# Performance work log

Hardware: AMD Instinct MI355X
Metric: run time of the kernel (lower is better)

## Reference

```python
import math
import jax, jax.numpy as jnp
import numpy as np

EMBED_DIM = 768
NUM_HEADS = 12
SCALE = 0.125
KERNEL_SIZE = 5
SIGMA = 1.0


def gaussian_kernel1d(ksize, sigma):
    x = jnp.arange(ksize, dtype=jnp.float32) - (ksize - 1) / 2.0
    g = jnp.exp(-0.5 * (x / sigma) ** 2)
    return g / g.sum()


def gaussian_blur_2d(x, ksize, sigma):
    # x: [N, C, P, P]; per-channel (depthwise) separable gaussian blur,
    # reflect padding, matching torchvision.transforms.functional.gaussian_blur.
    N, C, P, _ = x.shape
    g = gaussian_kernel1d(ksize, sigma)
    k2d = jnp.outer(g, g)[None, None]  # [1,1,k,k] (separable == full outer kernel)
    pad = ksize // 2
    xp = jnp.pad(x.reshape(N * C, 1, P, P), ((0, 0), (0, 0), (pad, pad), (pad, pad)), mode='reflect')
    y = jax.lax.conv_general_dilated(
        xp, k2d.astype(x.dtype), window_strides=(1, 1), padding='VALID',
        dimension_numbers=('NCHW', 'OIHW', 'NCHW'))
    return y.reshape(N, C, P, P)


def setup_inputs() -> dict:
    key = jax.random.key(0)
    k1, k2 = jax.random.split(key)
    B, S, E = 8, 1024, EMBED_DIM
    x = jax.random.normal(k1, (B, S, E), dtype=jnp.float32)
    # xavier_uniform for [3E, E]
    bound = math.sqrt(6.0 / (3 * E + E))
    W_in = jax.random.uniform(k2, (3 * E, E), dtype=jnp.float32, minval=-bound, maxval=bound)
    return {"x": x, "W_in": W_in}


def reference(x, W_in):
    B, S, E = x.shape
    H, D = NUM_HEADS, E // NUM_HEADS
    # fused QKV projection; chunk order is (values, keys, queries)
    qkv = jnp.einsum('bse,fe->bsf', x, W_in)  # [B, S, 3E]
    _v, k, q = jnp.split(qkv, 3, axis=-1)

    def to_heads(t):
        return t.reshape(B, S, H, D).transpose(0, 2, 1, 3).reshape(B * H, S, D)

    q, k = to_heads(q), to_heads(k)
    logits = SCALE * jnp.einsum('nqd,nkd->nqk', q, k)  # [B*H, S, S]
    P = int(math.sqrt(S))
    logits4 = logits.reshape(B * H, S, P, P)  # key axis viewed as PxP patch grid
    blurred = gaussian_blur_2d(logits4, KERNEL_SIZE, SIGMA)
    attn = jax.nn.softmax(blurred.reshape(B * H, S, S), axis=-1)
    return attn
```

## Files before the change

### kernel.cpp

```cpp
#include <hip/hip_runtime.h>


typedef __attribute__((ext_vector_type(8))) short short8;
typedef __attribute__((ext_vector_type(4))) float f32x4;

__device__ __forceinline__ float bf2f(unsigned short u) {
    unsigned int v = ((unsigned int)u) << 16;
    return __builtin_bit_cast(float, v);
}
__device__ __forceinline__ unsigned short f2bf(float f) {
    unsigned int u = __builtin_bit_cast(unsigned int, f);
    u += 0x7FFFu + ((u >> 16) & 1u);
    return (unsigned short)(u >> 16);
}

__device__ __forceinline__ void g2lds16(const unsigned short* g, unsigned short* l) {
    __builtin_amdgcn_global_load_lds(
        (const __attribute__((address_space(1))) void*)g,
        (__attribute__((address_space(3))) void*)l, 16, 0, 0);
}

#if defined(__has_builtin) && __has_builtin(__builtin_amdgcn_exp2f)
#define EXP2F(x) __builtin_amdgcn_exp2f(x)
#else
#define EXP2F(x) exp2f(x)
#endif

#define QSCALE 0.1803368801111204f

__global__ __launch_bounds__(256) void k_cast(const float* __restrict__ x,
                                              const float* __restrict__ w,
                                              unsigned short* __restrict__ dst) {
    const int NX = 8 * 1024 * 768;
    int i = (blockIdx.x * 256 + threadIdx.x) * 4;
    float4 v;
    if (i < NX) v = *(const float4*)(x + i);
    else        v = *(const float4*)(w + 768 * 768 + (i - NX));
    ushort4 o;
    o.x = f2bf(v.x); o.y = f2bf(v.y); o.z = f2bf(v.z); o.w = f2bf(v.w);
    *(ushort4*)(dst + i) = o;
}

__global__ __launch_bounds__(256) void k_proj(const unsigned short* __restrict__ xb,
                                              const unsigned short* __restrict__ wb,
                                              unsigned short* __restrict__ qh,
                                              unsigned short* __restrict__ kh) {
    __shared__ unsigned short As[128 * 64];
    __shared__ unsigned short Bs[128 * 64];

    const int lane = threadIdx.x & 63;
    const int wv   = threadIdx.x >> 6;
    const int m0   = blockIdx.x * 128;
    const int n0   = blockIdx.y * 128;
    const int col  = lane & 15;
    const int quad = lane >> 4;
    const int wm   = (wv >> 1) * 64;
    const int wn   = (wv & 1) * 64;

    const int srow   = wv * 32 + (lane >> 3);
    const int schunk = ((lane & 7) ^ ((lane >> 3) & 7)) * 8;
    const unsigned short* ag = xb + (size_t)(m0 + srow) * 768 + schunk;
    const unsigned short* bg = wb + (size_t)(n0 + srow) * 768 + schunk;
    unsigned short* al = As + (wv * 32) * 64;
    unsigned short* bl = Bs + (wv * 32) * 64;

    f32x4 acc[4][4] = {};

    for (int kk = 0; kk < 768; kk += 64) {
        __syncthreads();
#pragma unroll
        for (int j = 0; j < 4; ++j) {
            g2lds16(ag + j * 8 * 768 + kk, al + j * 8 * 64);
            g2lds16(bg + j * 8 * 768 + kk, bl + j * 8 * 64);
        }
        __syncthreads();

#pragma unroll
        for (int kc = 0; kc < 2; ++kc) {
            const int ch = ((kc * 4 + quad) ^ (col & 7)) * 8;
            short8 a[4], b[4];
#pragma unroll
            for (int mt = 0; mt < 4; ++mt)
                a[mt] = *(const short8*)(const void*)(As + (wm + mt * 16 + col) * 64 + ch);
#pragma unroll
            for (int nt = 0; nt < 4; ++nt)
                b[nt] = *(const short8*)(const void*)(Bs + (wn + nt * 16 + col) * 64 + ch);
#pragma unroll
            for (int mt = 0; mt < 4; ++mt)
#pragma unroll
                for (int nt = 0; nt < 4; ++nt)
                    acc[mt][nt] = __builtin_amdgcn_mfma_f32_16x16x32_bf16(
                        a[mt], b[nt], acc[mt][nt], 0, 0, 0);
        }
    }

#pragma unroll
    for (int nt = 0; nt < 4; ++nt) {
        int f = n0 + wn + nt * 16 + col;
        bool isq = (f >= 768);
        int fl = isq ? (f - 768) : f;
        int h = fl >> 6, d = fl & 63;
        unsigned short* dstb = isq ? qh : kh;
        float scl = isq ? QSCALE : 1.0f;
#pragma unroll
        for (int mt = 0; mt < 4; ++mt) {
#pragma unroll
            for (int i = 0; i < 4; ++i) {
                int t = m0 + wm + mt * 16 + quad * 4 + i;
                int n = (t >> 10) * 12 + h;
                dstb[((n << 10) + (t & 1023)) * 64 + d] = f2bf(acc[mt][nt][i] * scl);
            }
        }
    }
}

__global__ __launch_bounds__(256) void k_blurf(const unsigned short* __restrict__ src,
                                               unsigned short* __restrict__ dst) {
    __shared__ __align__(16) unsigned short sin_[12 * 32 * 16];
    __shared__ __align__(16) unsigned short stm_[8 * 32 * 16];

    const int tid = threadIdx.x;
    const int n   = blockIdx.y;
    const int rt  = blockIdx.x & 3;
    const int dc  = (blockIdx.x >> 2) * 16;
    const int r0  = rt * 8;
    const float g5[5] = {0.054488684f, 0.24420134f, 0.40261995f, 0.24420134f, 0.054488684f};

#pragma unroll
    for (int it = 0; it < 6; ++it) {
        int l   = it * 256 + tid;
        int row = l >> 7;
        int c   = (l >> 2) & 31;
        int gq  = l & 3;
        int pr  = r0 + row - 2;
        if (pr < 0)  pr = -pr;
        if (pr > 31) pr = 62 - pr;
        *(uint2*)(void*)(sin_ + ((row * 32 + c) << 4) + gq * 4) =
            *(const uint2*)(const void*)(src + (((size_t)n << 10) + pr * 32 + c) * 64 + dc + gq * 4);
    }
    __syncthreads();

#pragma unroll
    for (int it = 0; it < 4; ++it) {
        int l   = it * 256 + tid;
        int row = l >> 7;
        int c   = (l >> 2) & 31;
        int gq  = l & 3;
        float a0 = 0.f, a1 = 0.f, a2 = 0.f, a3 = 0.f;
#pragma unroll
        for (int o = 0; o < 5; ++o) {
            uint2 u = *(const uint2*)(const void*)(sin_ + (((row + o) * 32 + c) << 4) + gq * 4);
            float w = g5[o];
            a0 += w * bf2f((unsigned short)(u.x & 0xffff));
            a1 += w * bf2f((unsigned short)(u.x >> 16));
            a2 += w * bf2f((unsigned short)(u.y & 0xffff));
            a3 += w * bf2f((unsigned short)(u.y >> 16));
        }
        uint2 ov;
        ov.x = (unsigned)f2bf(a0) | ((unsigned)f2bf(a1) << 16);
        ov.y = (unsigned)f2bf(a2) | ((unsigned)f2bf(a3) << 16);
        *(uint2*)(void*)(stm_ + ((row * 32 + c) << 4) + gq * 4) = ov;
    }
    __syncthreads();

#pragma unroll
    for (int it = 0; it < 4; ++it) {
        int l   = it * 256 + tid;
        int row = l >> 7;
        int c   = (l >> 2) & 31;
        int gq  = l & 3;
        float a0 = 0.f, a1 = 0.f, a2 = 0.f, a3 = 0.f;
#pragma unroll
        for (int o = -2; o <= 2; ++o) {
            int pc = c + o;
            if (pc < 0)  pc = -pc;
            if (pc > 31) pc = 62 - pc;
            uint2 u = *(const uint2*)(const void*)(stm_ + ((row * 32 + pc) << 4) + gq * 4);
            float w = g5[o + 2];
            a0 += w * bf2f((unsigned short)(u.x & 0xffff));
            a1 += w * bf2f((unsigned short)(u.x >> 16));
            a2 += w * bf2f((unsigned short)(u.y & 0xffff));
            a3 += w * bf2f((unsigned short)(u.y >> 16));
        }
        uint2 ov;
        ov.x = (unsigned)f2bf(a0) | ((unsigned)f2bf(a1) << 16);
        ov.y = (unsigned)f2bf(a2) | ((unsigned)f2bf(a3) << 16);
        *(uint2*)(void*)(dst + (((size_t)n << 10) + (r0 + row) * 32 + c) * 64 + dc + gq * 4) = ov;
    }
}

__global__ __launch_bounds__(256) void k_attn(const unsigned short* __restrict__ qh,
                                              const unsigned short* __restrict__ kt,
                                              float* __restrict__ out) {
    const int lane = threadIdx.x & 63;
    const int wv   = threadIdx.x >> 6;
    const int n    = blockIdx.y;
    const int s0   = blockIdx.x * 16;
    const int col  = lane & 15;
    const int kq   = (lane >> 4) * 8;

    __shared__ float red[2][4][16];

    const unsigned short* qp = qh + ((n << 10) + s0 + col) * 64 + kq;
    short8 a0 = *(const short8*)(const void*)(qp);
    short8 a1 = *(const short8*)(const void*)(qp + 32);

    f32x4 acc[16];
    const unsigned short* kp = kt + ((n << 10) + wv * 256 + col) * 64 + kq;
#pragma unroll
    for (int t = 0; t < 16; ++t) {
        short8 b0 = *(const short8*)(const void*)(kp + t * 1024);
        short8 b1 = *(const short8*)(const void*)(kp + t * 1024 + 32);
        f32x4 c = {};
        c = __builtin_amdgcn_mfma_f32_16x16x32_bf16(a0, b0, c, 0, 0, 0);
        c = __builtin_amdgcn_mfma_f32_16x16x32_bf16(a1, b1, c, 0, 0, 0);
        acc[t] = c;
    }

    float mx[4];
#pragma unroll
    for (int i = 0; i < 4; ++i) {
        float m = acc[0][i];
#pragma unroll
        for (int t = 1; t < 16; ++t) m = fmaxf(m, acc[t][i]);
#pragma unroll
        for (int off = 1; off < 16; off <<= 1) m = fmaxf(m, __shfl_xor(m, off, 64));
        mx[i] = m;
    }
    if (col == 0) {
#pragma unroll
        for (int i = 0; i < 4; ++i) red[0][wv][(lane >> 4) * 4 + i] = mx[i];
    }
    __syncthreads();

    float sm[4];
#pragma unroll
    for (int i = 0; i < 4; ++i) {
        int qloc = (lane >> 4) * 4 + i;
        float m = fmaxf(fmaxf(red[0][0][qloc], red[0][1][qloc]),
                        fmaxf(red[0][2][qloc], red[0][3][qloc]));
        float s = 0.f;
#pragma unroll
        for (int t = 0; t < 16; ++t) {
            float e = EXP2F(acc[t][i] - m);
            acc[t][i] = e;
            s += e;
        }
#pragma unroll
        for (int off = 1; off < 16; off <<= 1) s += __shfl_xor(s, off, 64);
        sm[i] = s;
    }
    if (col == 0) {
#pragma unroll
        for (int i = 0; i < 4; ++i) red[1][wv][(lane >> 4) * 4 + i] = sm[i];
    }
    __syncthreads();

#pragma unroll
    for (int i = 0; i < 4; ++i) {
        int qloc = (lane >> 4) * 4 + i;
        float s = red[1][0][qloc] + red[1][1][qloc] + red[1][2][qloc] + red[1][3][qloc];
        float inv = 1.0f / s;
        float* op = out + (((size_t)(n << 10) + s0 + qloc) << 10) + wv * 256 + col;
#pragma unroll
        for (int t = 0; t < 16; ++t) op[t * 16] = acc[t][i] * inv;
    }
}

extern "C" void kernel_launch(void* const* d_in, const int* in_sizes, int n_in,
                              void* d_out, int out_size, void* d_ws, size_t ws_size,
                              hipStream_t stream) {
    const float* x = (const float*)d_in[0];
    const float* W = (const float*)d_in[1];
    float* out = (float*)d_out;

    unsigned short* ws   = (unsigned short*)d_ws;
    unsigned short* xb   = ws;
    unsigned short* wb   = xb + 6291456;
    unsigned short* qh   = wb + 1179648;
    unsigned short* kh   = qh + 6291456;
    unsigned short* kt   = kh + 6291456;

    k_cast<<<7296, 256, 0, stream>>>(x, W, xb);
    k_proj<<<dim3(64, 12), 256, 0, stream>>>(xb, wb, qh, kh);
    k_blurf<<<dim3(16, 96), 256, 0, stream>>>(kh, kt);
    k_attn<<<dim3(64, 96), 256, 0, stream>>>(qh, kt, out);
}
```

Baseline: 522.8 us.

## Fuse four kernels into one cooperative persistent kernel with grid syncs

Merges the cast, QKV projection, blur and attention/softmax kernels into a single cooperative kernel launched with 768 blocks. Stages are separated by grid-wide syncs, and blocks loop over the work of the blur and attention stages. This is meant to remove per-launch overhead and the gaps between kernels. In exchange it adds grid-sync cost, caps occupancy at 768 resident blocks (launch_bounds 256,3), and keeps the four-launch path as a fallback if the cooperative launch fails.

```diff
diff --git a/kernel.cpp b/kernel.cpp
--- a/kernel.cpp
+++ b/kernel.cpp
@@ -1,4 +1,7 @@
 #include <hip/hip_runtime.h>
+#include <hip/hip_cooperative_groups.h>
+
+namespace cg = cooperative_groups;
 
 
 typedef __attribute__((ext_vector_type(8))) short short8;
@@ -28,11 +31,11 @@
 
 #define QSCALE 0.1803368801111204f
 
-__global__ __launch_bounds__(256) void k_cast(const float* __restrict__ x,
-                                              const float* __restrict__ w,
-                                              unsigned short* __restrict__ dst) {
+
+__device__ __forceinline__ void cast_body(int i, const float* __restrict__ x,
+                                          const float* __restrict__ w,
+                                          unsigned short* __restrict__ dst) {
     const int NX = 8 * 1024 * 768;
-    int i = (blockIdx.x * 256 + threadIdx.x) * 4;
     float4 v;
     if (i < NX) v = *(const float4*)(x + i);
     else        v = *(const float4*)(w + 768 * 768 + (i - NX));
@@ -41,17 +44,16 @@
     *(ushort4*)(dst + i) = o;
 }
 
-__global__ __launch_bounds__(256) void k_proj(const unsigned short* __restrict__ xb,
-                                              const unsigned short* __restrict__ wb,
-                                              unsigned short* __restrict__ qh,
-                                              unsigned short* __restrict__ kh) {
-    __shared__ unsigned short As[128 * 64];
-    __shared__ unsigned short Bs[128 * 64];
-
-    const int lane = threadIdx.x & 63;
-    const int wv   = threadIdx.x >> 6;
-    const int m0   = blockIdx.x * 128;
-    const int n0   = blockIdx.y * 128;
+__device__ __forceinline__ void proj_body(int bx, int by, int tid,
+                                          unsigned short* As, unsigned short* Bs,
+                                          const unsigned short* __restrict__ xb,
+                                          const unsigned short* __restrict__ wb,
+                                          unsigned short* __restrict__ qh,
+                                          unsigned short* __restrict__ kh) {
+    const int lane = tid & 63;
+    const int wv   = tid >> 6;
+    const int m0   = bx * 128;
+    const int n0   = by * 128;
     const int col  = lane & 15;
     const int quad = lane >> 4;
     const int wm   = (wv >> 1) * 64;
@@ -114,15 +116,12 @@
     }
 }
 
-__global__ __launch_bounds__(256) void k_blurf(const unsigned short* __restrict__ src,
-                                               unsigned short* __restrict__ dst) {
-    __shared__ __align__(16) unsigned short sin_[12 * 32 * 16];
-    __shared__ __align__(16) unsigned short stm_[8 * 32 * 16];
-
-    const int tid = threadIdx.x;
-    const int n   = blockIdx.y;
-    const int rt  = blockIdx.x & 3;
-    const int dc  = (blockIdx.x >> 2) * 16;
+__device__ __forceinline__ void blur_body(int bxx, int n, int tid,
+                                          unsigned short* sin_, unsigned short* stm_,
+                                          const unsigned short* __restrict__ src,
+                                          unsigned short* __restrict__ dst) {
+    const int rt  = bxx & 3;
+    const int dc  = (bxx >> 2) * 16;
     const int r0  = rt * 8;
     const float g5[5] = {0.054488684f, 0.24420134f, 0.40261995f, 0.24420134f, 0.054488684f};
 
@@ -189,17 +188,17 @@
     }
 }
 
-__global__ __launch_bounds__(256) void k_attn(const unsigned short* __restrict__ qh,
-                                              const unsigned short* __restrict__ kt,
-                                              float* __restrict__ out) {
-    const int lane = threadIdx.x & 63;
-    const int wv   = threadIdx.x >> 6;
-    const int n    = blockIdx.y;
-    const int s0   = blockIdx.x * 16;
+__device__ __forceinline__ void attn_body(int s0, int n, int tid,
+                                          float* redf,
+                                          const unsigned short* __restrict__ qh,
+                                          const unsigned short* __restrict__ kt,
+                                          float* __restrict__ out) {
+    const int lane = tid & 63;
+    const int wv   = tid >> 6;
     const int col  = lane & 15;
     const int kq   = (lane >> 4) * 8;
 
-    __shared__ float red[2][4][16];
+#define RED(a, b, c) redf[((a) * 4 + (b)) * 16 + (c)]
 
     const unsigned short* qp = qh + ((n << 10) + s0 + col) * 64 + kq;
     short8 a0 = *(const short8*)(const void*)(qp);
@@ -229,7 +228,7 @@
     }
     if (col == 0) {
 #pragma unroll
-        for (int i = 0; i < 4; ++i) red[0][wv][(lane >> 4) * 4 + i] = mx[i];
+        for (int i = 0; i < 4; ++i) RED(0, wv, (lane >> 4) * 4 + i) = mx[i];
     }
     __syncthreads();
 
@@ -237,8 +236,8 @@
 #pragma unroll
     for (int i = 0; i < 4; ++i) {
         int qloc = (lane >> 4) * 4 + i;
-        float m = fmaxf(fmaxf(red[0][0][qloc], red[0][1][qloc]),
-                        fmaxf(red[0][2][qloc], red[0][3][qloc]));
+        float m = fmaxf(fmaxf(RED(0, 0, qloc), RED(0, 1, qloc)),
+                        fmaxf(RED(0, 2, qloc), RED(0, 3, qloc)));
         float s = 0.f;
 #pragma unroll
         for (int t = 0; t < 16; ++t) {
@@ -252,19 +251,85 @@
     }
     if (col == 0) {
 #pragma unroll
-        for (int i = 0; i < 4; ++i) red[1][wv][(lane >> 4) * 4 + i] = sm[i];
+        for (int i = 0; i < 4; ++i) RED(1, wv, (lane >> 4) * 4 + i) = sm[i];
     }
     __syncthreads();
 
 #pragma unroll
     for (int i = 0; i < 4; ++i) {
         int qloc = (lane >> 4) * 4 + i;
-        float s = red[1][0][qloc] + red[1][1][qloc] + red[1][2][qloc] + red[1][3][qloc];
+        float s = RED(1, 0, qloc) + RED(1, 1, qloc) + RED(1, 2, qloc) + RED(1, 3, qloc);
         float inv = 1.0f / s;
         float* op = out + (((size_t)(n << 10) + s0 + qloc) << 10) + wv * 256 + col;
 #pragma unroll
         for (int t = 0; t < 16; ++t) op[t * 16] = acc[t][i] * inv;
     }
+#undef RED
+}
+
+__global__ __launch_bounds__(256, 3) void k_mega(const float* __restrict__ x,
+                                                 const float* __restrict__ W,
+                                                 unsigned short* __restrict__ xb,
+                                                 unsigned short* __restrict__ wb,
+                                                 unsigned short* __restrict__ qh,
+                                                 unsigned short* __restrict__ kh,
+                                                 unsigned short* __restrict__ kt,
+                                                 float* __restrict__ out) {
+    __shared__ __align__(16) char smem[32768];
+    const int bid = blockIdx.x;
+    const int tid = threadIdx.x;
+    cg::grid_group grid = cg::this_grid();
+
+    {
+        const int TOT4 = 7471104 / 4;
+        for (int i4 = bid * 256 + tid; i4 < TOT4; i4 += 768 * 256)
+            cast_body(i4 * 4, x, W, xb);
+    }
+    grid.sync();
+
+    proj_body(bid & 63, bid >> 6, tid,
+              (unsigned short*)smem, (unsigned short*)(smem + 16384),
+              xb, wb, qh, kh);
+    grid.sync();
+
+    for (int vb = bid; vb < 1536; vb += 768)
+        blur_body(vb & 15, vb >> 4, tid,
+                  (unsigned short*)smem, (unsigned short*)(smem + 12288),
+                  kh, kt);
+    grid.sync();
+
+    for (int va = bid; va < 6144; va += 768)
+        attn_body((va & 63) * 16, va >> 6, tid, (float*)smem, qh, kt, out);
+}
+
+__global__ __launch_bounds__(256) void k_cast(const float* __restrict__ x,
+                                              const float* __restrict__ w,
+                                              unsigned short* __restrict__ dst) {
+    int i = (blockIdx.x * 256 + threadIdx.x) * 4;
+    cast_body(i, x, w, dst);
+}
+
+__global__ __launch_bounds__(256) void k_proj(const unsigned short* __restrict__ xb,
+                                              const unsigned short* __restrict__ wb,
+                                              unsigned short* __restrict__ qh,
+                                              unsigned short* __restrict__ kh) {
+    __shared__ __align__(16) unsigned short As[128 * 64];
+    __shared__ __align__(16) unsigned short Bs[128 * 64];
+    proj_body(blockIdx.x, blockIdx.y, threadIdx.x, As, Bs, xb, wb, qh, kh);
+}
+
+__global__ __launch_bounds__(256) void k_blurf(const unsigned short* __restrict__ src,
+                                               unsigned short* __restrict__ dst) {
+    __shared__ __align__(16) unsigned short sin_[12 * 32 * 16];
+    __shared__ __align__(16) unsigned short stm_[8 * 32 * 16];
+    blur_body(blockIdx.x, blockIdx.y, threadIdx.x, sin_, stm_, src, dst);
+}
+
+__global__ __launch_bounds__(256) void k_attn(const unsigned short* __restrict__ qh,
+                                              const unsigned short* __restrict__ kt,
+                                              float* __restrict__ out) {
+    __shared__ __align__(16) float red[2 * 4 * 16];
+    attn_body(blockIdx.x * 16, blockIdx.y, threadIdx.x, red, qh, kt, out);
 }
 
 extern "C" void kernel_launch(void* const* d_in, const int* in_sizes, int n_in,
@@ -281,8 +346,15 @@
     unsigned short* kh   = qh + 6291456;
     unsigned short* kt   = kh + 6291456;
 
-    k_cast<<<7296, 256, 0, stream>>>(x, W, xb);
-    k_proj<<<dim3(64, 12), 256, 0, stream>>>(xb, wb, qh, kh);
-    k_blurf<<<dim3(16, 96), 256, 0, stream>>>(kh, kt);
-    k_attn<<<dim3(64, 96), 256, 0, stream>>>(qh, kt, out);
-}
+    void* args[] = {(void*)&x, (void*)&W, (void*)&xb, (void*)&wb,
+                    (void*)&qh, (void*)&kh, (void*)&kt, (void*)&out};
+    hipError_t err = hipLaunchCooperativeKernel((const void*)k_mega,
+                                                dim3(768), dim3(256),
+                                                args, 0, stream);
+    if (err != hipSuccess) {
+        k_cast<<<7296, 256, 0, stream>>>(x, W, xb);
+        k_proj<<<dim3(64, 12), 256, 0, stream>>>(xb, wb, qh, kh);
+        k_blurf<<<dim3(16, 96), 256, 0, stream>>>(kh, kt);
+        k_attn<<<dim3(64, 96), 256, 0, stream>>>(qh, kt, out);
+    }
+}
```

After: 764.4 us. 1.46x slower.
